# Optimization experiments

Measured on AMD Instinct MI355X. Metric: run time of the kernel, lower is better.

The kernel has to match this reference:

```python
import jax, jax.numpy as jnp
import numpy as np

B, F, H, E, O = 512, 512, 512, 8, 512  # batch, feature, hidden, experts, out_frame


def setup_inputs() -> dict:
    key = jax.random.key(0)
    ks = jax.random.split(key, 14)
    u = lambda k, shape, s: jax.random.uniform(k, shape, jnp.float32) * s
    return {
        "x": jax.random.normal(ks[0], (B, F), jnp.float32),
        # gating MLP params (torch Linear: y = x @ W.T + b)
        "gw0": u(ks[1], (H, F), 0.04) - 0.02,
        "gb0": jnp.zeros((H,), jnp.float32),
        "gw1": u(ks[2], (H, H), 0.04) - 0.02,
        "gb1": jnp.zeros((H,), jnp.float32),
        "gw2": u(ks[3], (E, H), 0.04) - 0.02,
        "gb2": jnp.zeros((E,), jnp.float32),
        # expert weight/bias banks
        "alpha0": u(ks[4], (E, H, F), 0.01),
        "beta0": jnp.zeros((E, H, 1), jnp.float32),
        "alpha1": u(ks[5], (E, H, H), 0.01),
        "beta1": jnp.zeros((E, H, 1), jnp.float32),
        "alpha2": u(ks[6], (E, O, H), 0.01),
        "beta2": jnp.zeros((E, O, 1), jnp.float32),
    }


def reference(x, gw0, gb0, gw1, gb1, gw2, gb2,
              alpha0, beta0, alpha1, beta1, alpha2, beta2):
    # gating network
    h = jax.nn.elu(x @ gw0.T + gb0)
    h = jax.nn.elu(h @ gw1.T + gb1)
    g = jax.nn.softmax(h @ gw2.T + gb2, axis=1)  # [B, E]

    # per-sample blended weights (sum over experts of gate-scaled expert mats)
    blend_w = lambda a: jnp.einsum('be,ehf->bhf', g, a)
    blend_b = lambda b: jnp.einsum('be,eh->bh', g, b[..., 0])

    # per-sample 3-layer MLP (bmm with vector rhs == batched matvec)
    H1 = jax.nn.elu(jnp.einsum('bhf,bf->bh', blend_w(alpha0), x) + blend_b(beta0))
    H2 = jax.nn.elu(jnp.einsum('bhf,bf->bh', blend_w(alpha1), H1) + blend_b(beta1))
    H3 = jnp.einsum('bof,bf->bo', blend_w(alpha2), H2) + blend_b(beta2)
    return H3
```

## Files before the change

### kernel.cpp

```cpp
#include <hip/hip_runtime.h>
#include <hip/hip_bf16.h>
#include <math.h>

enum { Bq = 512, Fq = 512, Hq = 512, Eq = 8, Oq = 512 };

typedef __attribute__((ext_vector_type(8))) short short8;
typedef __attribute__((ext_vector_type(4))) float floatx4;

static __device__ __forceinline__ unsigned short f2bf(float f) {
  unsigned u = __float_as_uint(f);
  u += 0x7fffu + ((u >> 16) & 1u);
  return (unsigned short)(u >> 16);
}
static __device__ __forceinline__ float bf2f(unsigned short h) {
  return __uint_as_float(((unsigned)h) << 16);
}
static __device__ __forceinline__ float elu1(float v) {
  return v > 0.f ? v : (__expf(v) - 1.f);
}

typedef __attribute__((address_space(1))) const unsigned int gu32;
typedef __attribute__((address_space(3))) unsigned int lu32;
static __device__ __forceinline__ void gld16(const unsigned short* g,
                                             unsigned short* l) {
  __builtin_amdgcn_global_load_lds((gu32*)g, (lu32*)l, 16, 0, 0);
}

static __device__ __forceinline__ int swz(int q, int r) {
  return (q & ~7) | ((q ^ r) & 7);
}

__global__ __launch_bounds__(256) void cvt6_kernel(
    const float* __restrict__ b0, const float* __restrict__ b1,
    const float* __restrict__ b2, unsigned short* __restrict__ db0,
    unsigned short* __restrict__ db1, unsigned short* __restrict__ db2,
    const float* __restrict__ s0, const float* __restrict__ s1,
    const float* __restrict__ s2, unsigned short* __restrict__ ds0,
    unsigned short* __restrict__ ds1, unsigned short* __restrict__ ds2,
    int nb, int ns) {
  int i = blockIdx.x * 256 + threadIdx.x;
  const float4* s;
  unsigned short* d;
  int j;
  if (i < 3 * nb) {
    int seg = i / nb;
    j = i - seg * nb;
    s = (seg == 0) ? (const float4*)b0
      : (seg == 1) ? (const float4*)b1 : (const float4*)b2;
    d = (seg == 0) ? db0 : (seg == 1) ? db1 : db2;
  } else {
    int k = i - 3 * nb;
    if (k >= 3 * ns) return;
    int seg = k / ns;
    j = k - seg * ns;
    s = (seg == 0) ? (const float4*)s0
      : (seg == 1) ? (const float4*)s1 : (const float4*)s2;
    d = (seg == 0) ? ds0 : (seg == 1) ? ds1 : ds2;
  }
  float4 v = s[j];
  ushort4 o;
  o.x = f2bf(v.x); o.y = f2bf(v.y); o.z = f2bf(v.z); o.w = f2bf(v.w);
  *(ushort4*)(d + 4 * (size_t)j) = o;
}

__global__ __launch_bounds__(256) void gating_gemm(
    const unsigned short* __restrict__ A, const unsigned short* __restrict__ W,
    const float* __restrict__ bias, unsigned short* __restrict__ C) {
  __shared__ unsigned short As[32 * 512];
  __shared__ unsigned short Ws[32 * 512];
  const int tid = threadIdx.x;
  const int wave = tid >> 6, lane = tid & 63;
  const int wm = wave >> 1, wn = wave & 1;
  const int lr = lane & 15, lk = lane >> 4;
  const int m0 = blockIdx.y * 32, n0 = blockIdx.x * 32;
#pragma unroll
  for (int i = 0; i < 8; i++) {
    int c = tid + i * 256;
    int r = c >> 6, ql = c & 63;
    gld16(&A[(size_t)(m0 + r) * 512 + swz(ql, r) * 8], &As[(c & ~63) * 8]);
  }
#pragma unroll
  for (int i = 0; i < 8; i++) {
    int c = tid + i * 256;
    int r = c >> 6, ql = c & 63;
    gld16(&W[(size_t)(n0 + r) * 512 + swz(ql, r) * 8], &Ws[(c & ~63) * 8]);
  }
  __syncthreads();
  const int rA = wm * 16 + lr, rB = wn * 16 + lr;
  floatx4 ac[4];
#pragma unroll
  for (int j = 0; j < 4; j++) ac[j] = (floatx4){0.f, 0.f, 0.f, 0.f};
#pragma unroll
  for (int t = 0; t < 4; t++) {
#pragma unroll
    for (int j = 0; j < 4; j++) {
      int q = ((j * 128 + t * 32) >> 3) + lk;
      short8 av = *(const short8*)&As[rA * 512 + swz(q, rA) * 8];
      short8 bv = *(const short8*)&Ws[rB * 512 + swz(q, rB) * 8];
      ac[j] = __builtin_amdgcn_mfma_f32_16x16x32_bf16(av, bv, ac[j], 0, 0, 0);
    }
  }
  floatx4 acc = (ac[0] + ac[1]) + (ac[2] + ac[3]);
  int n = n0 + wn * 16 + lr;
  float bn = bias[n];
#pragma unroll
  for (int r = 0; r < 4; r++) {
    int m = m0 + wm * 16 + lk * 4 + r;
    C[(size_t)m * 512 + n] = f2bf(elu1(acc[r] + bn));
  }
}

template <int FROMP>
__global__ __launch_bounds__(256) void expert_gemm(
    const unsigned short* __restrict__ A,
    const float* __restrict__ Pin,
    const unsigned short* __restrict__ Wb,
    const float* __restrict__ g,
    const float* __restrict__ beta,
    float* __restrict__ Pout) {
  __shared__ unsigned short As[64 * 128];
  __shared__ unsigned short Ws[3][64 * 128];
  __shared__ float gl[64 * 8];
  const int tid = threadIdx.x;
  const int wave = tid >> 6, lane = tid & 63;
  const int wm = wave >> 1, wn = wave & 1;
  const int lr = lane & 15, lk = lane >> 4;
  const int n0 = blockIdx.x * 64, m0 = blockIdx.y * 64;
  const int kz = blockIdx.z, kbeg = kz * 128;

  if (FROMP) {
#pragma unroll
    for (int i = 0; i < 4; i++) {
      int c = tid + i * 256;
      int r = c >> 4, q = c & 15;
      const float* p = Pin + (size_t)(m0 + r) * 512 + kbeg + q * 8;
      float s0 = 0.f, s1 = 0.f, s2 = 0.f, s3 = 0.f;
      float s4 = 0.f, s5 = 0.f, s6 = 0.f, s7 = 0.f;
#pragma unroll
      for (int z = 0; z < 4; z++) {
        const float* pz = p + (size_t)z * (Bq * Hq);
        float4 a = *(const float4*)pz;
        float4 b = *(const float4*)(pz + 4);
        s0 += a.x; s1 += a.y; s2 += a.z; s3 += a.w;
        s4 += b.x; s5 += b.y; s6 += b.z; s7 += b.w;
      }
      short8 o;
      o[0] = (short)f2bf(elu1(s0)); o[1] = (short)f2bf(elu1(s1));
      o[2] = (short)f2bf(elu1(s2)); o[3] = (short)f2bf(elu1(s3));
      o[4] = (short)f2bf(elu1(s4)); o[5] = (short)f2bf(elu1(s5));
      o[6] = (short)f2bf(elu1(s6)); o[7] = (short)f2bf(elu1(s7));
      *(short8*)&As[(r * 16 + swz(q, r)) * 8] = o;
    }
  } else {
#pragma unroll
    for (int i = 0; i < 4; i++) {
      int c = tid + i * 256;
      int r = c >> 4, ql = c & 15;
      gld16(&A[(size_t)(m0 + r) * 512 + kbeg + swz(ql, r) * 8],
            &As[(c & ~63) * 8]);
    }
  }
  if (tid < 128)
    ((float4*)gl)[tid] = ((const float4*)(g + (size_t)m0 * 8))[tid];

  auto stageW = [&](int e, int b) {
    const unsigned short* Wp = Wb + ((size_t)e * 512 + n0) * 512 + kbeg;
#pragma unroll
    for (int i = 0; i < 4; i++) {
      int c = tid + i * 256;
      int r = c >> 4, ql = c & 15;
      gld16(&Wp[(size_t)r * 512 + swz(ql, r) * 8], &Ws[b][(c & ~63) * 8]);
    }
  };
  stageW(0, 0);
  stageW(1, 1);

  const int rA0 = wm * 32 + lr, rB0 = wn * 32 + lr;
  short8 af[2][4];
  floatx4 fin[2][2];
#pragma unroll
  for (int i = 0; i < 2; i++)
#pragma unroll
    for (int j = 0; j < 2; j++) fin[i][j] = (floatx4){0.f, 0.f, 0.f, 0.f};

#pragma unroll
  for (int e = 0; e < 8; e++) {
    if (e == 0)
      __builtin_amdgcn_s_waitcnt(0x0074);
    else if (e < 7)
      __builtin_amdgcn_s_waitcnt(0x0F74);
    else
      __builtin_amdgcn_s_waitcnt(0x0F70);
    __builtin_amdgcn_s_barrier();
    if (e + 2 < 8) stageW(e + 2, (e + 2) % 3);
    if (e == 0) {
#pragma unroll
      for (int i = 0; i < 2; i++) {
        int r = rA0 + i * 16;
#pragma unroll
        for (int t = 0; t < 4; t++)
          af[i][t] = *(const short8*)&As[r * 128 + swz(t * 4 + lk, r) * 8];
      }
    }
    const unsigned short* wb = Ws[e % 3];
    floatx4 acc[2][2];
#pragma unroll
    for (int i = 0; i < 2; i++)
#pragma unroll
      for (int j = 0; j < 2; j++) acc[i][j] = (floatx4){0.f, 0.f, 0.f, 0.f};
#pragma unroll
    for (int t = 0; t < 4; t++) {
      short8 bf[2];
#pragma unroll
      for (int j = 0; j < 2; j++) {
        int r = rB0 + j * 16;
        bf[j] = *(const short8*)&wb[r * 128 + swz(t * 4 + lk, r) * 8];
      }
#pragma unroll
      for (int i = 0; i < 2; i++)
#pragma unroll
        for (int j = 0; j < 2; j++)
          acc[i][j] = __builtin_amdgcn_mfma_f32_16x16x32_bf16(
              af[i][t], bf[j], acc[i][j], 0, 0, 0);
    }
#pragma unroll
    for (int i = 0; i < 2; i++) {
#pragma unroll
      for (int r = 0; r < 4; r++) {
        float ge = gl[(wm * 32 + i * 16 + lk * 4 + r) * 8 + e];
#pragma unroll
        for (int j = 0; j < 2; j++) fin[i][j][r] += ge * acc[i][j][r];
      }
    }
  }

  float* Po = Pout + (size_t)kz * Bq * Hq;
#pragma unroll
  for (int i = 0; i < 2; i++) {
#pragma unroll
    for (int j = 0; j < 2; j++) {
      int n = n0 + wn * 32 + j * 16 + lr;
#pragma unroll
      for (int r = 0; r < 4; r++) {
        int m = m0 + wm * 32 + i * 16 + lk * 4 + r;
        float v = fin[i][j][r];
        if (kz == 0) {
#pragma unroll
          for (int e = 0; e < 8; e++)
            v += gl[(wm * 32 + i * 16 + lk * 4 + r) * 8 + e] *
                 beta[e * 512 + n];
        }
        Po[(size_t)m * 512 + n] = v;
      }
    }
  }
}

__global__ __launch_bounds__(64) void gate_kernel(
    const unsigned short* __restrict__ G1,
    const float* __restrict__ gw2,
    const float* __restrict__ gb2,
    float* __restrict__ g) {
  int b = blockIdx.x;
  int lane = threadIdx.x;
  float xv[8];
#pragma unroll
  for (int t = 0; t < 8; t++) xv[t] = bf2f(G1[(size_t)b * Hq + t * 64 + lane]);
  float le[Eq];
#pragma unroll
  for (int e = 0; e < Eq; e++) {
    float p = 0.f;
#pragma unroll
    for (int t = 0; t < 8; t++)
      p += xv[t] * gw2[(size_t)e * Hq + t * 64 + lane];
#pragma unroll
    for (int o = 32; o > 0; o >>= 1) p += __shfl_xor(p, o);
    le[e] = p + gb2[e];
  }
  float m = le[0];
#pragma unroll
  for (int e = 1; e < Eq; e++) m = fmaxf(m, le[e]);
  float s = 0.f;
#pragma unroll
  for (int e = 0; e < Eq; e++) {
    le[e] = __expf(le[e] - m);
    s += le[e];
  }
  float inv = 1.f / s;
  if (lane == 0) {
#pragma unroll
    for (int e = 0; e < Eq; e++) g[(size_t)b * Eq + e] = le[e] * inv;
  }
}

__global__ __launch_bounds__(256) void reduce_final(
    const float* __restrict__ P, float* __restrict__ outf) {
  int idx = blockIdx.x * 256 + threadIdx.x;
  float4 s = {0.f, 0.f, 0.f, 0.f};
#pragma unroll
  for (int z = 0; z < 4; z++) {
    float4 v = ((const float4*)(P + (size_t)z * Bq * Hq))[idx];
    s.x += v.x; s.y += v.y; s.z += v.z; s.w += v.w;
  }
  ((float4*)outf)[idx] = s;
}

extern "C" void kernel_launch(void* const* d_in, const int* in_sizes, int n_in,
                              void* d_out, int out_size, void* d_ws,
                              size_t ws_size, hipStream_t stream) {
  const float* x = (const float*)d_in[0];
  const float* gw0 = (const float*)d_in[1];
  const float* gb0 = (const float*)d_in[2];
  const float* gw1 = (const float*)d_in[3];
  const float* gb1 = (const float*)d_in[4];
  const float* gw2 = (const float*)d_in[5];
  const float* gb2 = (const float*)d_in[6];
  const float* alpha0 = (const float*)d_in[7];
  const float* beta0 = (const float*)d_in[8];
  const float* alpha1 = (const float*)d_in[9];
  const float* beta1 = (const float*)d_in[10];
  const float* alpha2 = (const float*)d_in[11];
  const float* beta2 = (const float*)d_in[12];
  float* out = (float*)d_out;

  char* ws = (char*)d_ws;
  auto alloc = [&](size_t bytes) {
    char* p = ws;
    ws += (bytes + 255) & ~(size_t)255;
    return p;
  };
  unsigned short* xb = (unsigned short*)alloc((size_t)Bq * Fq * 2);
  unsigned short* gw0b = (unsigned short*)alloc((size_t)Hq * Fq * 2);
  unsigned short* gw1b = (unsigned short*)alloc((size_t)Hq * Hq * 2);
  unsigned short* a0b = (unsigned short*)alloc((size_t)Eq * Hq * Fq * 2);
  unsigned short* a1b = (unsigned short*)alloc((size_t)Eq * Hq * Hq * 2);
  unsigned short* a2b = (unsigned short*)alloc((size_t)Eq * Oq * Hq * 2);
  unsigned short* G0b = (unsigned short*)alloc((size_t)Bq * Hq * 2);
  unsigned short* G1b = (unsigned short*)alloc((size_t)Bq * Hq * 2);
  float* gates = (float*)alloc((size_t)Bq * Eq * 4);
  float* P1 = (float*)alloc((size_t)4 * Bq * Hq * 4);
  float* P2 = (float*)alloc((size_t)4 * Bq * Hq * 4);

  {
    int nb = (Eq * Hq * Fq) / 4, ns = (Bq * Fq) / 4;
    int total = 3 * nb + 3 * ns;
    cvt6_kernel<<<(total + 255) / 256, 256, 0, stream>>>(
        alpha0, alpha1, alpha2, a0b, a1b, a2b, x, gw0, gw1, xb, gw0b, gw1b,
        nb, ns);
  }

  dim3 gg(16, 16);
  gating_gemm<<<gg, 256, 0, stream>>>(xb, gw0b, gb0, G0b);
  gating_gemm<<<gg, 256, 0, stream>>>(G0b, gw1b, gb1, G1b);

  gate_kernel<<<Bq, 64, 0, stream>>>(G1b, gw2, gb2, gates);

  dim3 ge(8, 8, 4);
  expert_gemm<0><<<ge, 256, 0, stream>>>(xb, nullptr, a0b, gates, beta0, P1);
  expert_gemm<1><<<ge, 256, 0, stream>>>(nullptr, P1, a1b, gates, beta1, P2);
  expert_gemm<1><<<ge, 256, 0, stream>>>(nullptr, P2, a2b, gates, beta2, P1);
  reduce_final<<<(Bq * Hq / 4) / 256, 256, 0, stream>>>(P1, out);
}
```

Measured before the change: 142.9 us.

## Halve expert GEMM N-tile to 32 and simplify to double-buffered weight staging

The expert GEMM tile shrinks from 64x64 to 64x32 outputs per block, doubling the grid to 16x8x4 = 512 blocks so more of the GPU's compute units have work. Weight staging moves from a triple buffer with hand-tuned waitcnt to a double buffer with __syncthreads, and LDS use drops. Each wave now issues two MFMAs per k-step instead of four. The A tile and gates are loaded, and for the FROMP layers the partial sums reduced, twice as often across blocks, and the simpler sync may expose load latency.

```diff
diff --git a/kernel.cpp b/kernel.cpp
--- a/kernel.cpp
+++ b/kernel.cpp
@@ -119,13 +119,13 @@
     const float* __restrict__ beta,
     float* __restrict__ Pout) {
   __shared__ unsigned short As[64 * 128];
-  __shared__ unsigned short Ws[3][64 * 128];
+  __shared__ unsigned short Ws[2][32 * 128];
   __shared__ float gl[64 * 8];
   const int tid = threadIdx.x;
   const int wave = tid >> 6, lane = tid & 63;
   const int wm = wave >> 1, wn = wave & 1;
   const int lr = lane & 15, lk = lane >> 4;
-  const int n0 = blockIdx.x * 64, m0 = blockIdx.y * 64;
+  const int n0 = blockIdx.x * 32, m0 = blockIdx.y * 64;
   const int kz = blockIdx.z, kbeg = kz * 128;
 
   if (FROMP) {
@@ -166,92 +166,65 @@
   auto stageW = [&](int e, int b) {
     const unsigned short* Wp = Wb + ((size_t)e * 512 + n0) * 512 + kbeg;
 #pragma unroll
-    for (int i = 0; i < 4; i++) {
+    for (int i = 0; i < 2; i++) {
       int c = tid + i * 256;
       int r = c >> 4, ql = c & 15;
       gld16(&Wp[(size_t)r * 512 + swz(ql, r) * 8], &Ws[b][(c & ~63) * 8]);
     }
   };
   stageW(0, 0);
-  stageW(1, 1);
-
-  const int rA0 = wm * 32 + lr, rB0 = wn * 32 + lr;
+
   short8 af[2][4];
-  floatx4 fin[2][2];
-#pragma unroll
-  for (int i = 0; i < 2; i++)
-#pragma unroll
-    for (int j = 0; j < 2; j++) fin[i][j] = (floatx4){0.f, 0.f, 0.f, 0.f};
+  floatx4 fin[2] = {{0.f, 0.f, 0.f, 0.f}, {0.f, 0.f, 0.f, 0.f}};
+  const int rB = wn * 16 + lr;
 
 #pragma unroll
   for (int e = 0; e < 8; e++) {
-    if (e == 0)
-      __builtin_amdgcn_s_waitcnt(0x0074);
-    else if (e < 7)
-      __builtin_amdgcn_s_waitcnt(0x0F74);
-    else
-      __builtin_amdgcn_s_waitcnt(0x0F70);
-    __builtin_amdgcn_s_barrier();
-    if (e + 2 < 8) stageW(e + 2, (e + 2) % 3);
+    __syncthreads();
+    if (e < 7) stageW(e + 1, (e + 1) & 1);
     if (e == 0) {
 #pragma unroll
-      for (int i = 0; i < 2; i++) {
-        int r = rA0 + i * 16;
+      for (int s = 0; s < 2; s++) {
+        int rA = s * 32 + wm * 16 + lr;
 #pragma unroll
         for (int t = 0; t < 4; t++)
-          af[i][t] = *(const short8*)&As[r * 128 + swz(t * 4 + lk, r) * 8];
+          af[s][t] = *(const short8*)&As[(rA * 16 + swz(t * 4 + lk, rA)) * 8];
       }
     }
-    const unsigned short* wb = Ws[e % 3];
-    floatx4 acc[2][2];
-#pragma unroll
-    for (int i = 0; i < 2; i++)
-#pragma unroll
-      for (int j = 0; j < 2; j++) acc[i][j] = (floatx4){0.f, 0.f, 0.f, 0.f};
+    const unsigned short* wb = Ws[e & 1];
+    floatx4 acc[2] = {{0.f, 0.f, 0.f, 0.f}, {0.f, 0.f, 0.f, 0.f}};
 #pragma unroll
     for (int t = 0; t < 4; t++) {
-      short8 bf[2];
-#pragma unroll
-      for (int j = 0; j < 2; j++) {
-        int r = rB0 + j * 16;
-        bf[j] = *(const short8*)&wb[r * 128 + swz(t * 4 + lk, r) * 8];
+      short8 bv = *(const short8*)&wb[(rB * 16 + swz(t * 4 + lk, rB)) * 8];
+      acc[0] = __builtin_amdgcn_mfma_f32_16x16x32_bf16(af[0][t], bv, acc[0],
+                                                       0, 0, 0);
+      acc[1] = __builtin_amdgcn_mfma_f32_16x16x32_bf16(af[1][t], bv, acc[1],
+                                                       0, 0, 0);
+    }
+#pragma unroll
+    for (int s = 0; s < 2; s++) {
+#pragma unroll
+      for (int r = 0; r < 4; r++) {
+        float ge = gl[(s * 32 + wm * 16 + lk * 4 + r) * 8 + e];
+        fin[s][r] += ge * acc[s][r];
       }
-#pragma unroll
-      for (int i = 0; i < 2; i++)
-#pragma unroll
-        for (int j = 0; j < 2; j++)
-          acc[i][j] = __builtin_amdgcn_mfma_f32_16x16x32_bf16(
-              af[i][t], bf[j], acc[i][j], 0, 0, 0);
-    }
-#pragma unroll
-    for (int i = 0; i < 2; i++) {
-#pragma unroll
-      for (int r = 0; r < 4; r++) {
-        float ge = gl[(wm * 32 + i * 16 + lk * 4 + r) * 8 + e];
-#pragma unroll
-        for (int j = 0; j < 2; j++) fin[i][j][r] += ge * acc[i][j][r];
+    }
+  }
+
+  float* Po = Pout + (size_t)kz * Bq * Hq;
+  int n = n0 + wn * 16 + lr;
+#pragma unroll
+  for (int s = 0; s < 2; s++) {
+#pragma unroll
+    for (int r = 0; r < 4; r++) {
+      int row = s * 32 + wm * 16 + lk * 4 + r;
+      float v = fin[s][r];
+      if (kz == 0) {
+#pragma unroll
+        for (int e = 0; e < 8; e++)
+          v += gl[row * 8 + e] * beta[e * 512 + n];
       }
-    }
-  }
-
-  float* Po = Pout + (size_t)kz * Bq * Hq;
-#pragma unroll
-  for (int i = 0; i < 2; i++) {
-#pragma unroll
-    for (int j = 0; j < 2; j++) {
-      int n = n0 + wn * 32 + j * 16 + lr;
-#pragma unroll
-      for (int r = 0; r < 4; r++) {
-        int m = m0 + wm * 32 + i * 16 + lk * 4 + r;
-        float v = fin[i][j][r];
-        if (kz == 0) {
-#pragma unroll
-          for (int e = 0; e < 8; e++)
-            v += gl[(wm * 32 + i * 16 + lk * 4 + r) * 8 + e] *
-                 beta[e * 512 + n];
-        }
-        Po[(size_t)m * 512 + n] = v;
-      }
+      Po[(size_t)(m0 + row) * 512 + n] = v;
     }
   }
 }
@@ -355,7 +328,7 @@
 
   gate_kernel<<<Bq, 64, 0, stream>>>(G1b, gw2, gb2, gates);
 
-  dim3 ge(8, 8, 4);
+  dim3 ge(16, 8, 4);
   expert_gemm<0><<<ge, 256, 0, stream>>>(xb, nullptr, a0b, gates, beta0, P1);
   expert_gemm<1><<<ge, 256, 0, stream>>>(nullptr, P1, a1b, gates, beta1, P2);
   expert_gemm<1><<<ge, 256, 0, stream>>>(nullptr, P2, a2b, gates, beta2, P1);
```

Result: faster. 139.2 us (-2.6%).
